# Kernel tuning notes

Measured on AMD Instinct MI355X. Metric: run time of the kernel, lower is better.

The kernel has to match this reference:

```python
import jax, jax.numpy as jnp
import numpy as np

S, B, D, F, E, K = 1024, 2, 512, 2048, 8, 2


def setup_inputs() -> dict:
    key = jax.random.key(0)
    ks = jax.random.split(key, 12)
    s = lambda *sh: 1.0 / np.sqrt(sh[0])
    inp = {
        "x": jax.random.normal(ks[0], (S, B, D), dtype=jnp.float32),
        # gate: nn.Linear(d_model, n_experts)
        "Wg": jax.random.normal(ks[1], (D, E), dtype=jnp.float32) * s(D),
        "bg": jnp.zeros((E,), dtype=jnp.float32),
        # routed experts: stacked FFN params (E copies of expert)
        "W1": jax.random.normal(ks[2], (E, D, F), dtype=jnp.float32) * s(D),
        "b1": jnp.zeros((E, F), dtype=jnp.float32),
        "W2": jax.random.normal(ks[3], (E, F, D), dtype=jnp.float32) * s(F),
        "b2": jnp.zeros((E, D), dtype=jnp.float32),
        # shared expert (single FFN)
        "Ws1": jax.random.normal(ks[4], (D, F), dtype=jnp.float32) * s(D),
        "bs1": jnp.zeros((F,), dtype=jnp.float32),
        "Ws2": jax.random.normal(ks[5], (F, D), dtype=jnp.float32) * s(F),
        "bs2": jnp.zeros((D,), dtype=jnp.float32),
    }
    return inp


def reference(x, Wg, bg, W1, b1, W2, b2, Ws1, bs1, Ws2, bs2):
    # gate_logits: (S, B, E)
    gate_logits = jnp.einsum("sbd,de->sbe", x, Wg) + bg
    # top-k per token (eval mode: k = n_experts_per_token, t = 1.0)
    weights, selected = jax.lax.top_k(gate_logits, K)  # (S,B,K)
    weights = jax.nn.softmax(weights.astype(jnp.float32), axis=-1)
    # combine weights per expert: (S,B,E)
    onehot = jax.nn.one_hot(selected, E, dtype=weights.dtype)  # (S,B,K,E)
    comb = jnp.einsum("sbk,sbke->sbe", weights, onehot)
    # routed experts computed densely, combined with per-token routing weight
    h = jax.nn.relu(jnp.einsum("sbd,edf->sbef", x, W1) + b1)  # (S,B,E,F)
    y = jnp.einsum("sbef,efd->sbed", h, W2) + b2              # (S,B,E,D)
    out = jnp.einsum("sbe,sbed->sbd", comb, y)
    # shared expert, scaled by 1/k
    hs = jax.nn.relu(jnp.einsum("sbd,df->sbf", x, Ws1) + bs1)
    shared = jnp.einsum("sbf,fd->sbd", hs, Ws2) + bs2
    out = out + (1.0 / K) * shared
    return out
```

## Files before the change

### kernel.cpp

```cpp
#include <hip/hip_runtime.h>
#include <hip/hip_bf16.h>
#include <stdint.h>

#define TT 2048
#define DD 512
#define FF 2048
#define EE 8

typedef unsigned short u16;
typedef __attribute__((ext_vector_type(8))) unsigned short ushort8v;
typedef __attribute__((ext_vector_type(8))) short short8;
typedef __attribute__((ext_vector_type(4))) float float4v;

__device__ __forceinline__ u16 f2bf(float f) {
    unsigned u = __float_as_uint(f);
    u += 0x7FFF + ((u >> 16) & 1);
    return (u16)(u >> 16);
}

__device__ __forceinline__ void gl_lds16(const u16* g, u16* l) {
    __builtin_amdgcn_global_load_lds(
        (const __attribute__((address_space(1))) unsigned int*)g,
        (__attribute__((address_space(3))) unsigned int*)l, 16, 0, 0);
}

#define WS_HB   0ull
#define WS_XG   (WS_HB + 6144ull*2048*2)
#define WS_WT1  (WS_XG + 2048ull*512*2)
#define WS_ME   (WS_WT1 + 9ull*2048*512*2)
#define WS_MW   (WS_ME + 16384)
#define WS_RT   (WS_MW + 16384)
#define WS_WROW (WS_RT + 16384)
#define WS_TROW (WS_WROW + 16384)
#define WS_RTG  (WS_TROW + 16384)
#define WS_WT2  (WS_RTG + 128)
#define WS_YB   (WS_WT2 + 9ull*2048*512*2)
#define YS      (6144ull*512)
#define WS_NEED (WS_YB + 2ull*6144*512*4)

__device__ __forceinline__ void conv_unit(int j, const float* __restrict__ srcE,
                                          const float* __restrict__ srcS,
                                          u16* __restrict__ dst,
                                          int R, int C, int shC, u16* Ls) {
    int mid = j >> 8, t2 = j & 255;
    int tr = t2 >> shC, tc = t2 & ((1 << shC) - 1);
    int r0 = tr * 64, c0 = tc * 64;
    const float* src = (mid < 8) ? srcE + (size_t)mid * R * C : srcS;
    u16* dstm = dst + (size_t)mid * R * C;
    int t = threadIdx.x;
#pragma unroll
    for (int i = 0; i < 4; ++i) {
        int rr = (t >> 4) + i * 16;
        int cc = (t & 15) * 4;
        float4v v = *(const float4v*)(src + (size_t)(r0 + rr) * C + c0 + cc);
#pragma unroll
        for (int jx = 0; jx < 4; ++jx) Ls[(cc + jx) * 72 + rr] = f2bf(v[jx]);
    }
    __syncthreads();
#pragma unroll
    for (int jj = 0; jj < 2; ++jj) {
        int slot = t + jj * 256;
        int cc = slot >> 3, r8 = (slot & 7) * 8;
        ushort8v o = *(const ushort8v*)&Ls[cc * 72 + r8];
        *(ushort8v*)(dstm + (size_t)(c0 + cc) * R + r0 + r8) = o;
    }
}

__device__ __forceinline__ void gate_wave(int t, int lane,
                                          const float* __restrict__ x,
                                          const float* __restrict__ Wg,
                                          const float* __restrict__ bg,
                                          int* __restrict__ metaE,
                                          float* __restrict__ metaW,
                                          u16* __restrict__ xg) {
    const float* xp = x + (size_t)t * DD + lane * 8;
    float4v x0 = *(const float4v*)xp;
    float4v x1 = *(const float4v*)(xp + 4);
    float xf[8] = {x0[0], x0[1], x0[2], x0[3], x1[0], x1[1], x1[2], x1[3]};
    float acc[EE] = {0.f, 0.f, 0.f, 0.f, 0.f, 0.f, 0.f, 0.f};
#pragma unroll
    for (int g = 0; g < 8; ++g) {
        const float* wp = Wg + (size_t)(lane * 8 + g) * EE;
        float4v w0 = *(const float4v*)wp;
        float4v w1 = *(const float4v*)(wp + 4);
        acc[0] += xf[g] * w0[0]; acc[1] += xf[g] * w0[1];
        acc[2] += xf[g] * w0[2]; acc[3] += xf[g] * w0[3];
        acc[4] += xf[g] * w1[0]; acc[5] += xf[g] * w1[1];
        acc[6] += xf[g] * w1[2]; acc[7] += xf[g] * w1[3];
    }
#pragma unroll
    for (int off = 1; off < 64; off <<= 1) {
#pragma unroll
        for (int e = 0; e < EE; ++e) acc[e] += __shfl_xor(acc[e], off, 64);
    }
    ushort8v xv;
#pragma unroll
    for (int jx = 0; jx < 4; ++jx) xv[jx] = f2bf(x0[jx]);
#pragma unroll
    for (int jx = 0; jx < 4; ++jx) xv[4 + jx] = f2bf(x1[jx]);
    *(ushort8v*)(xg + (size_t)t * DD + lane * 8) = xv;
    if (lane == 0) {
#pragma unroll
        for (int e = 0; e < EE; ++e) acc[e] += bg[e];
        int e0 = 0; float l0 = acc[0];
#pragma unroll
        for (int e = 1; e < EE; ++e) if (acc[e] > l0) { l0 = acc[e]; e0 = e; }
        int e1 = -1; float l1 = -3.4e38f;
#pragma unroll
        for (int e = 0; e < EE; ++e)
            if (e != e0 && acc[e] > l1) { l1 = acc[e]; e1 = e; }
        float ex = __expf(l1 - l0);
        float w0 = 1.f / (1.f + ex);
        metaE[2 * t] = e0; metaE[2 * t + 1] = e1;
        metaW[2 * t] = w0; metaW[2 * t + 1] = 1.f - w0;
    }
}

__global__ __launch_bounds__(256) void fused1_k(
    const float* __restrict__ x, const float* __restrict__ Wg,
    const float* __restrict__ bg,
    const float* __restrict__ W1, const float* __restrict__ Ws1,
    const float* __restrict__ W2, const float* __restrict__ Ws2,
    float* __restrict__ out, u16* __restrict__ xg,
    u16* __restrict__ Wt1, u16* __restrict__ Wt2,
    int* __restrict__ metaE, float* __restrict__ metaW, int nconv) {
    __shared__ __align__(16) u16 Ls[64 * 72];
    int b = blockIdx.x, tid = threadIdx.x;
    if (b < nconv) {
        if (b < 2304) conv_unit(b, W1, Ws1, Wt1, DD, FF, 5, Ls);
        else          conv_unit(b - 2304, W2, Ws2, Wt2, FF, DD, 3, Ls);
    } else if (b < nconv + 512) {
        int gb = b - nconv;
        gate_wave(gb * 4 + (tid >> 6), tid & 63, x, Wg, bg, metaE, metaW, xg);
    } else {
        int zb = b - nconv - 512;
        float* op = out + (size_t)zb * 8192;
#pragma unroll
        for (int it = 0; it < 8; ++it)
            *(float4v*)(op + it * 1024 + tid * 4) = (float4v){0.f, 0.f, 0.f, 0.f};
    }
}

__global__ __launch_bounds__(256) void conv2_k(const float* __restrict__ W2,
                                               const float* __restrict__ Ws2,
                                               u16* __restrict__ Wt2) {
    __shared__ __align__(16) u16 Ls[64 * 72];
    conv_unit(blockIdx.x, W2, Ws2, Wt2, FF, DD, 3, Ls);
}

__global__ __launch_bounds__(256) void rank_k(const int* __restrict__ metaE,
                                              const float* __restrict__ metaW,
                                              int* __restrict__ routing,
                                              int* __restrict__ rtok,
                                              float* __restrict__ wrow,
                                              int* __restrict__ trow) {
    __shared__ __align__(16) char smem[16384];
    u16* er      = (u16*)smem;
    int* segCnt  = (int*)(smem + 8192);
    int* segBase = (int*)(smem + 10240);
    int* expTot  = (int*)(smem + 12288);
    int tid = threadIdx.x, wv = tid >> 6, lane = tid & 63;
    unsigned long long below = (lane == 0) ? 0ull : ((~0ull) >> (64 - lane));
    for (int s = wv * 16; s < wv * 16 + 16; ++s) {
        int entry = s * 64 + lane;
        int e = metaE[entry];
        int rk = 0;
#pragma unroll
        for (int ee = 0; ee < 8; ++ee) {
            unsigned long long m = __ballot(e == ee);
            if (e == ee) rk = __popcll(m & below);
            if (lane == ee) segCnt[s * 8 + ee] = __popcll(m);
        }
        er[entry] = (u16)(e | (rk << 4));
    }
    __syncthreads();
    if (tid < 8) {
        int s = 0;
        for (int g = 0; g < 64; ++g) { segBase[g * 8 + tid] = s; s += segCnt[g * 8 + tid]; }
        expTot[tid] = s;
    }
    __syncthreads();
    if (tid == 0) {
        int s = 0;
        for (int e = 0; e < 8; ++e) { int c = expTot[e]; expTot[8 + e] = s; s += c; }
    }
    __syncthreads();
    if (tid < 8) { routing[tid] = expTot[8 + tid]; routing[8 + tid] = expTot[tid]; }
    for (int i = 0; i < 16; ++i) {
        int entry = tid + i * 256;
        int v = er[entry];
        int e = v & 15, rk = v >> 4;
        int row = expTot[8 + e] + segBase[(entry >> 6) * 8 + e] + rk;
        rtok[row] = entry >> 1;
        wrow[row] = metaW[entry];
        trow[entry] = row;
    }
}

__global__ __launch_bounds__(256) void gemmA_k(
    const u16* __restrict__ xg, const u16* __restrict__ Wt1,
    const float* __restrict__ b1, const float* __restrict__ bs1,
    const int* __restrict__ routing, const int* __restrict__ rtok,
    u16* __restrict__ hbuf,
    const float* __restrict__ W2, const float* __restrict__ Ws2,
    u16* __restrict__ Wt2, int ncv) {
    __shared__ __align__(16) u16 SM[12288];
    int j = blockIdx.x, tid = threadIdx.x;
    if (j < ncv) { conv_unit(j, W2, Ws2, Wt2, FF, DD, 3, SM); return; }
    j -= ncv;
    u16* As = SM;
    u16* Bs = SM + 4096;
    const int* offs = routing; const int* cnt = routing + 8;
    int rt, ct, Mloc, hRowBase, rowBase; bool routed;
    const u16* Bsrc; const float* bias;
    if (j < 512) {
        rt = j >> 4; ct = j & 15; Mloc = 64; rowBase = rt * 64;
        Bsrc = Wt1 + (size_t)8 * FF * DD; bias = bs1;
        hRowBase = 4096 + rt * 64; routed = false;
    } else {
        int jr = j - 512; int e = jr & 7; int rc = jr >> 3;
        rt = rc >> 4; ct = rc & 15;
        int M = cnt[e]; if (rt * 64 >= M) return;
        Mloc = M - rt * 64; if (Mloc > 64) Mloc = 64;
        rowBase = offs[e] + rt * 64;
        Bsrc = Wt1 + (size_t)e * FF * DD; bias = b1 + e * FF;
        hRowBase = rowBase; routed = true;
    }
    int n0 = ct * 128;
    int lane = tid & 63, w = tid >> 6, ln = lane & 15, quad = lane >> 4;
    int wm = w >> 1, wn = w & 1;
    int lr8 = lane >> 3;
    int cs = (lane & 7) ^ lr8;
    const u16* ApS[2];
#pragma unroll
    for (int i = 0; i < 2; ++i) {
        int r = w * 16 + i * 8 + lr8;
        int tok;
        if (routed) { int br = rowBase + r; if (br > 4095) br = 4095; tok = rtok[br]; }
        else tok = rowBase + r;
        ApS[i] = xg + (size_t)tok * DD + cs * 8;
    }
    const u16* BpS[4];
#pragma unroll
    for (int i = 0; i < 4; ++i) {
        int r = w * 32 + i * 8 + lr8;
        BpS[i] = Bsrc + (size_t)(n0 + r) * DD + cs * 8;
    }
    float4v acc[2][4];
#pragma unroll
    for (int a = 0; a < 2; ++a)
#pragma unroll
        for (int b = 0; b < 4; ++b) acc[a][b] = (float4v){0.f, 0.f, 0.f, 0.f};

#pragma unroll
    for (int kt = 0; kt < 8; ++kt) {
#pragma unroll
        for (int i = 0; i < 2; ++i)
            gl_lds16(ApS[i] + kt * 64, As + (w * 16 + i * 8) * 64);
#pragma unroll
        for (int i = 0; i < 4; ++i)
            gl_lds16(BpS[i] + kt * 64, Bs + (w * 32 + i * 8) * 64);
        asm volatile("s_waitcnt vmcnt(0)" ::: "memory");
        __builtin_amdgcn_s_barrier();
#pragma unroll
        for (int s = 0; s < 2; ++s) {
            int chs = ((s * 4 + quad) ^ (ln & 7)) * 8;
            short8 Af[2], Bf[4];
#pragma unroll
            for (int a = 0; a < 2; ++a) {
                int ra = wm * 32 + a * 16 + ln;
                Af[a] = *(const short8*)(As + ra * 64 + chs);
            }
#pragma unroll
            for (int b = 0; b < 4; ++b) {
                int rb = wn * 64 + b * 16 + ln;
                Bf[b] = *(const short8*)(Bs + rb * 64 + chs);
            }
#pragma unroll
            for (int a = 0; a < 2; ++a)
#pragma unroll
                for (int b = 0; b < 4; ++b)
                    acc[a][b] = __builtin_amdgcn_mfma_f32_16x16x32_bf16(Af[a], Bf[b], acc[a][b], 0, 0, 0);
        }
        __builtin_amdgcn_s_barrier();
    }
#pragma unroll
    for (int b = 0; b < 4; ++b) {
        int n = n0 + wn * 64 + b * 16 + ln;
        float bv = bias[n];
#pragma unroll
        for (int a = 0; a < 2; ++a) {
#pragma unroll
            for (int i = 0; i < 4; ++i) {
                int lr = wm * 32 + a * 16 + quad * 4 + i;
                if (lr < Mloc) {
                    float v = acc[a][b][i] + bv;
                    v = v > 0.f ? v : 0.f;
                    hbuf[(size_t)(hRowBase + lr) * FF + n] = f2bf(v);
                }
            }
        }
    }
}

__global__ __launch_bounds__(256) void gemmB_k(
    const u16* __restrict__ hbuf, const u16* __restrict__ Wt2,
    const float* __restrict__ b2, const float* __restrict__ bs2,
    const int* __restrict__ routing, float* __restrict__ ybuf) {
    __shared__ __align__(16) u16 SM[12288];
    u16* As = SM;
    u16* Bs = SM + 4096;
    const int* offs = routing; const int* cnt = routing + 8;
    int j = blockIdx.x, tid = threadIdx.x;
    int rt, ct, ks, Mloc, aRowBase;
    const u16* Bsrc; const float* bias;
    if (j < 256) {
        rt = j >> 3; ct = (j >> 1) & 3; ks = j & 1;
        Mloc = 64; aRowBase = 4096 + rt * 64;
        Bsrc = Wt2 + (size_t)8 * DD * FF; bias = bs2;
    } else {
        int jr = j - 256; int e = jr & 7; int rc = jr >> 3;
        ks = rc & 1; ct = (rc >> 1) & 3; rt = rc >> 3;
        int M = cnt[e]; if (rt * 64 >= M) return;
        Mloc = M - rt * 64; if (Mloc > 64) Mloc = 64;
        aRowBase = offs[e] + rt * 64;
        Bsrc = Wt2 + (size_t)e * DD * FF; bias = b2 + e * DD;
    }
    int n0 = ct * 128;
    int lane = tid & 63, w = tid >> 6, ln = lane & 15, quad = lane >> 4;
    int wm = w >> 1, wn = w & 1;
    int lr8 = lane >> 3;
    int cs = (lane & 7) ^ lr8;
    const u16* ApS[2];
#pragma unroll
    for (int i = 0; i < 2; ++i) {
        int r = w * 16 + i * 8 + lr8;
        ApS[i] = hbuf + (size_t)(aRowBase + r) * FF + ks * 1024 + cs * 8;
    }
    const u16* BpS[4];
#pragma unroll
    for (int i = 0; i < 4; ++i) {
        int r = w * 32 + i * 8 + lr8;
        BpS[i] = Bsrc + (size_t)(n0 + r) * FF + ks * 1024 + cs * 8;
    }
    float4v acc[2][4];
#pragma unroll
    for (int a = 0; a < 2; ++a)
#pragma unroll
        for (int b = 0; b < 4; ++b) acc[a][b] = (float4v){0.f, 0.f, 0.f, 0.f};

#pragma unroll
    for (int kt = 0; kt < 16; ++kt) {
#pragma unroll
        for (int i = 0; i < 2; ++i)
            gl_lds16(ApS[i] + kt * 64, As + (w * 16 + i * 8) * 64);
#pragma unroll
        for (int i = 0; i < 4; ++i)
            gl_lds16(BpS[i] + kt * 64, Bs + (w * 32 + i * 8) * 64);
        asm volatile("s_waitcnt vmcnt(0)" ::: "memory");
        __builtin_amdgcn_s_barrier();
#pragma unroll
        for (int s = 0; s < 2; ++s) {
            int chs = ((s * 4 + quad) ^ (ln & 7)) * 8;
            short8 Af[2], Bf[4];
#pragma unroll
            for (int a = 0; a < 2; ++a) {
                int ra = wm * 32 + a * 16 + ln;
                Af[a] = *(const short8*)(As + ra * 64 + chs);
            }
#pragma unroll
            for (int b = 0; b < 4; ++b) {
                int rb = wn * 64 + b * 16 + ln;
                Bf[b] = *(const short8*)(Bs + rb * 64 + chs);
            }
#pragma unroll
            for (int a = 0; a < 2; ++a)
#pragma unroll
                for (int b = 0; b < 4; ++b)
                    acc[a][b] = __builtin_amdgcn_mfma_f32_16x16x32_bf16(Af[a], Bf[b], acc[a][b], 0, 0, 0);
        }
        __builtin_amdgcn_s_barrier();
    }
    float* yb = ybuf + (size_t)ks * YS;
#pragma unroll
    for (int b = 0; b < 4; ++b) {
        int n = n0 + wn * 64 + b * 16 + ln;
        float bv = (ks == 0) ? bias[n] : 0.f;
#pragma unroll
        for (int a = 0; a < 2; ++a) {
#pragma unroll
            for (int i = 0; i < 4; ++i) {
                int lr = wm * 32 + a * 16 + quad * 4 + i;
                if (lr < Mloc)
                    yb[(size_t)(aRowBase + lr) * DD + n] = acc[a][b][i] + bv;
            }
        }
    }
}

__global__ __launch_bounds__(256) void combine_k(
    const float* __restrict__ ybuf, const int* __restrict__ trow,
    const float* __restrict__ metaW, float* __restrict__ out) {
    int tid = threadIdx.x;
    int tok = blockIdx.x * 2 + (tid >> 7);
    int q = (tid & 127) * 4;
    int r0 = trow[2 * tok], r1 = trow[2 * tok + 1];
    float w0 = metaW[2 * tok], w1 = metaW[2 * tok + 1];
    const float* ya = ybuf;
    const float* yb = ybuf + YS;
    float4v y0a = *(const float4v*)(ya + (size_t)r0 * DD + q);
    float4v y0b = *(const float4v*)(yb + (size_t)r0 * DD + q);
    float4v y1a = *(const float4v*)(ya + (size_t)r1 * DD + q);
    float4v y1b = *(const float4v*)(yb + (size_t)r1 * DD + q);
    float4v ysa = *(const float4v*)(ya + (size_t)(4096 + tok) * DD + q);
    float4v ysb = *(const float4v*)(yb + (size_t)(4096 + tok) * DD + q);
    float4v o;
#pragma unroll
    for (int i = 0; i < 4; ++i)
        o[i] = w0 * (y0a[i] + y0b[i]) + w1 * (y1a[i] + y1b[i]) + 0.5f * (ysa[i] + ysb[i]);
    *(float4v*)(out + (size_t)tok * DD + q) = o;
}

__global__ __launch_bounds__(256) void gemmBat_k(
    const u16* __restrict__ hbuf, const u16* __restrict__ Wt2,
    const float* __restrict__ b2, const float* __restrict__ bs2,
    const int* __restrict__ routing, const int* __restrict__ rtok,
    const float* __restrict__ wrow, float* __restrict__ out) {
    __shared__ __align__(16) u16 As[2][64 * 64];
    __shared__ __align__(16) u16 Bs[2][128 * 64];
    const int* offs = routing; const int* cnt = routing + 8;
    int j = blockIdx.x, tid = threadIdx.x;
    int rt, ct, ks, Mloc, aRowBase; bool sh;
    const u16* Bsrc; const float* bias;
    if (j < 256) {
        sh = true; rt = j >> 3; int sub = j & 7; ct = sub >> 1; ks = sub & 1;
        Mloc = 64; aRowBase = 4096 + rt * 64;
        Bsrc = Wt2 + (size_t)8 * DD * FF; bias = bs2;
    } else {
        sh = false; int jr = j - 256; int e = jr & 7; int rc = jr >> 3;
        rt = rc >> 3; ct = (rc >> 1) & 3; ks = rc & 1;
        int M = cnt[e]; if (rt * 64 >= M) return;
        Mloc = M - rt * 64; if (Mloc > 64) Mloc = 64;
        aRowBase = offs[e] + rt * 64;
        Bsrc = Wt2 + (size_t)e * DD * FF; bias = b2 + e * DD;
    }
    int n0 = ct * 128;
    int lane = tid & 63, w = tid >> 6, ln = lane & 15, quad = lane >> 4;
    int lr8 = lane >> 3;
    int cs = (lane & 7) ^ lr8;
    const u16* ApS[2];
#pragma unroll
    for (int i = 0; i < 2; ++i) {
        int r = w * 16 + i * 8 + lr8;
        ApS[i] = hbuf + (size_t)(aRowBase + r) * FF + ks * 1024 + cs * 8;
    }
    const u16* BpS[4];
#pragma unroll
    for (int i = 0; i < 4; ++i) {
        int r = w * 32 + i * 8 + lr8;
        BpS[i] = Bsrc + (size_t)(n0 + r) * FF + ks * 1024 + cs * 8;
    }
    float4v acc[2][4];
#pragma unroll
    for (int a = 0; a < 2; ++a)
#pragma unroll
        for (int b = 0; b < 4; ++b) acc[a][b] = (float4v){0.f, 0.f, 0.f, 0.f};
    auto stage = [&](int kt, int pb) {
        u16* Ab = &As[pb][0]; u16* Bb = &Bs[pb][0];
#pragma unroll
        for (int i = 0; i < 2; ++i)
            gl_lds16(ApS[i] + kt * 64, Ab + (w * 16 + i * 8) * 64);
#pragma unroll
        for (int i = 0; i < 4; ++i)
            gl_lds16(BpS[i] + kt * 64, Bb + (w * 32 + i * 8) * 64);
    };
    stage(0, 0);
#pragma unroll
    for (int kt = 0; kt < 16; ++kt) {
        int pb = kt & 1;
        if (kt < 15) {
            stage(kt + 1, pb ^ 1);
            asm volatile("s_waitcnt vmcnt(6)" ::: "memory");
        } else {
            asm volatile("s_waitcnt vmcnt(0)" ::: "memory");
        }
        __builtin_amdgcn_s_barrier();
        __builtin_amdgcn_sched_barrier(0);
        const u16* Ab = &As[pb][0]; const u16* Bb = &Bs[pb][0];
#pragma unroll
        for (int s = 0; s < 2; ++s) {
            int chs = ((s * 4 + quad) ^ (ln & 7)) * 8;
            short8 Af[2], Bf[4];
#pragma unroll
            for (int a = 0; a < 2; ++a) {
                int ra = (w & 1) * 32 + a * 16 + ln;
                Af[a] = *(const short8*)(Ab + ra * 64 + chs);
            }
#pragma unroll
            for (int b = 0; b < 4; ++b) {
                int rb = (w >> 1) * 64 + b * 16 + ln;
                Bf[b] = *(const short8*)(Bb + rb * 64 + chs);
            }
#pragma unroll
            for (int a = 0; a < 2; ++a)
#pragma unroll
                for (int b = 0; b < 4; ++b)
                    acc[a][b] = __builtin_amdgcn_mfma_f32_16x16x32_bf16(Af[a], Bf[b], acc[a][b], 0, 0, 0);
        }
        __builtin_amdgcn_sched_barrier(0);
        __builtin_amdgcn_s_barrier();
    }
    float bv[4];
#pragma unroll
    for (int b = 0; b < 4; ++b)
        bv[b] = (ks == 0) ? bias[n0 + (w >> 1) * 64 + b * 16 + ln] : 0.f;
#pragma unroll
    for (int a = 0; a < 2; ++a) {
#pragma unroll
        for (int i = 0; i < 4; ++i) {
            int lr = (w & 1) * 32 + a * 16 + quad * 4 + i;
            if (lr < Mloc) {
                int row = aRowBase + lr;
                int t; float wr;
                if (sh) { t = row - 4096; wr = 0.5f; }
                else    { t = rtok[row]; wr = wrow[row]; }
                float* op = out + (size_t)t * DD;
#pragma unroll
                for (int b = 0; b < 4; ++b) {
                    int n = n0 + (w >> 1) * 64 + b * 16 + ln;
                    atomicAdd(op + n, wr * (acc[a][b][i] + bv[b]));
                }
            }
        }
    }
}

extern "C" void kernel_launch(void* const* d_in, const int* in_sizes, int n_in,
                              void* d_out, int out_size, void* d_ws, size_t ws_size,
                              hipStream_t stream) {
    const float* x   = (const float*)d_in[0];
    const float* Wg  = (const float*)d_in[1];
    const float* bg  = (const float*)d_in[2];
    const float* W1  = (const float*)d_in[3];
    const float* b1  = (const float*)d_in[4];
    const float* W2  = (const float*)d_in[5];
    const float* b2  = (const float*)d_in[6];
    const float* Ws1 = (const float*)d_in[7];
    const float* bs1 = (const float*)d_in[8];
    const float* Ws2 = (const float*)d_in[9];
    const float* bs2 = (const float*)d_in[10];
    float* out = (float*)d_out;

    char* ws = (char*)d_ws;
    u16*   hbuf    = (u16*)(ws + WS_HB);
    u16*   xg      = (u16*)(ws + WS_XG);
    u16*   Wt1     = (u16*)(ws + WS_WT1);
    int*   metaE   = (int*)(ws + WS_ME);
    float* metaW   = (float*)(ws + WS_MW);
    int*   rtok    = (int*)(ws + WS_RT);
    float* wrow    = (float*)(ws + WS_WROW);
    int*   trow    = (int*)(ws + WS_TROW);
    int*   routing = (int*)(ws + WS_RTG);
    bool   big     = ws_size >= WS_NEED;
    u16*   Wt2     = big ? (u16*)(ws + WS_WT2) : Wt1;
    float* ybuf    = (float*)(ws + WS_YB);

    if (big) {
        fused1_k<<<2816, 256, 0, stream>>>(x, Wg, bg, W1, Ws1, W2, Ws2,
                                           out, xg, Wt1, Wt2, metaE, metaW, 2304);
        rank_k<<<1, 256, 0, stream>>>(metaE, metaW, routing, rtok, wrow, trow);
        gemmA_k<<<2304 + 512 + 8192, 256, 0, stream>>>(
            xg, Wt1, b1, bs1, routing, rtok, hbuf, W2, Ws2, Wt2, 2304);
        gemmB_k<<<256 + 4096, 256, 0, stream>>>(hbuf, Wt2, b2, bs2, routing, ybuf);
        combine_k<<<1024, 256, 0, stream>>>(ybuf, trow, metaW, out);
    } else {
        fused1_k<<<2944, 256, 0, stream>>>(x, Wg, bg, W1, Ws1, W2, Ws2,
                                           out, xg, Wt1, Wt2, metaE, metaW, 2304);
        rank_k<<<1, 256, 0, stream>>>(metaE, metaW, routing, rtok, wrow, trow);
        gemmA_k<<<512 + 8192, 256, 0, stream>>>(
            xg, Wt1, b1, bs1, routing, rtok, hbuf, W2, Ws2, Wt2, 0);
        conv2_k<<<2304, 256, 0, stream>>>(W2, Ws2, Wt2);
        gemmBat_k<<<4352, 256, 0, stream>>>(hbuf, Wt2, b2, bs2, routing, rtok, wrow, out);
    }
}
```

Before: 208.6 us.

## Drop split-K in second expert GEMM and double-buffer its LDS tiles

The second GEMM no longer splits K across two blocks writing separate partial buffers. Each block now loops over the full K with a double-buffered LDS prefetch (waiting on vmcnt(6) so the next tile's loads overlap the current MFMAs), and combine reads one partial instead of two. The weight-conversion transpose also changes its float loads from 4-wide vectors to strided scalars to reduce LDS bank conflicts. This halves the block count and the y-buffer traffic, at the cost of less parallelism per tile and doubled LDS use per block.

```diff
diff --git a/kernel.cpp b/kernel.cpp
--- a/kernel.cpp
+++ b/kernel.cpp
@@ -48,21 +48,22 @@
     const float* src = (mid < 8) ? srcE + (size_t)mid * R * C : srcS;
     u16* dstm = dst + (size_t)mid * R * C;
     int t = threadIdx.x;
+    int cc = t & 15, rbase = t >> 4;
 #pragma unroll
     for (int i = 0; i < 4; ++i) {
-        int rr = (t >> 4) + i * 16;
-        int cc = (t & 15) * 4;
-        float4v v = *(const float4v*)(src + (size_t)(r0 + rr) * C + c0 + cc);
-#pragma unroll
-        for (int jx = 0; jx < 4; ++jx) Ls[(cc + jx) * 72 + rr] = f2bf(v[jx]);
+        int rr = rbase + i * 16;
+        const float* sp = src + (size_t)(r0 + rr) * C + c0 + cc;
+#pragma unroll
+        for (int jx = 0; jx < 4; ++jx)
+            Ls[(cc + 16 * jx) * 72 + rr] = f2bf(sp[16 * jx]);
     }
     __syncthreads();
 #pragma unroll
     for (int jj = 0; jj < 2; ++jj) {
         int slot = t + jj * 256;
-        int cc = slot >> 3, r8 = (slot & 7) * 8;
-        ushort8v o = *(const ushort8v*)&Ls[cc * 72 + r8];
-        *(ushort8v*)(dstm + (size_t)(c0 + cc) * R + r0 + r8) = o;
+        int c2 = slot >> 3, r8 = (slot & 7) * 8;
+        ushort8v o = *(const ushort8v*)&Ls[c2 * 72 + r8];
+        *(ushort8v*)(dstm + (size_t)(c0 + c2) * R + r0 + r8) = o;
     }
 }
 
@@ -307,20 +308,19 @@
     const u16* __restrict__ hbuf, const u16* __restrict__ Wt2,
     const float* __restrict__ b2, const float* __restrict__ bs2,
     const int* __restrict__ routing, float* __restrict__ ybuf) {
-    __shared__ __align__(16) u16 SM[12288];
-    u16* As = SM;
-    u16* Bs = SM + 4096;
+    __shared__ __align__(16) u16 As[2][64 * 64];
+    __shared__ __align__(16) u16 Bs[2][128 * 64];
     const int* offs = routing; const int* cnt = routing + 8;
     int j = blockIdx.x, tid = threadIdx.x;
-    int rt, ct, ks, Mloc, aRowBase;
+    int rt, ct, Mloc, aRowBase;
     const u16* Bsrc; const float* bias;
-    if (j < 256) {
-        rt = j >> 3; ct = (j >> 1) & 3; ks = j & 1;
+    if (j < 128) {
+        rt = j >> 2; ct = j & 3;
         Mloc = 64; aRowBase = 4096 + rt * 64;
         Bsrc = Wt2 + (size_t)8 * DD * FF; bias = bs2;
     } else {
-        int jr = j - 256; int e = jr & 7; int rc = jr >> 3;
-        ks = rc & 1; ct = (rc >> 1) & 3; rt = rc >> 3;
+        int jr = j - 128; int e = jr & 7; int rc = jr >> 3;
+        rt = rc >> 2; ct = rc & 3;
         int M = cnt[e]; if (rt * 64 >= M) return;
         Mloc = M - rt * 64; if (Mloc > 64) Mloc = 64;
         aRowBase = offs[e] + rt * 64;
@@ -328,50 +328,60 @@
     }
     int n0 = ct * 128;
     int lane = tid & 63, w = tid >> 6, ln = lane & 15, quad = lane >> 4;
-    int wm = w >> 1, wn = w & 1;
     int lr8 = lane >> 3;
     int cs = (lane & 7) ^ lr8;
     const u16* ApS[2];
 #pragma unroll
     for (int i = 0; i < 2; ++i) {
         int r = w * 16 + i * 8 + lr8;
-        ApS[i] = hbuf + (size_t)(aRowBase + r) * FF + ks * 1024 + cs * 8;
+        ApS[i] = hbuf + (size_t)(aRowBase + r) * FF + cs * 8;
     }
     const u16* BpS[4];
 #pragma unroll
     for (int i = 0; i < 4; ++i) {
         int r = w * 32 + i * 8 + lr8;
-        BpS[i] = Bsrc + (size_t)(n0 + r) * FF + ks * 1024 + cs * 8;
+        BpS[i] = Bsrc + (size_t)(n0 + r) * FF + cs * 8;
     }
     float4v acc[2][4];
 #pragma unroll
     for (int a = 0; a < 2; ++a)
 #pragma unroll
         for (int b = 0; b < 4; ++b) acc[a][b] = (float4v){0.f, 0.f, 0.f, 0.f};
-
-#pragma unroll
-    for (int kt = 0; kt < 16; ++kt) {
+    auto stage = [&](int kt, int pb) {
+        u16* Ab = &As[pb][0]; u16* Bb = &Bs[pb][0];
 #pragma unroll
         for (int i = 0; i < 2; ++i)
-            gl_lds16(ApS[i] + kt * 64, As + (w * 16 + i * 8) * 64);
+            gl_lds16(ApS[i] + kt * 64, Ab + (w * 16 + i * 8) * 64);
 #pragma unroll
         for (int i = 0; i < 4; ++i)
-            gl_lds16(BpS[i] + kt * 64, Bs + (w * 32 + i * 8) * 64);
-        asm volatile("s_waitcnt vmcnt(0)" ::: "memory");
+            gl_lds16(BpS[i] + kt * 64, Bb + (w * 32 + i * 8) * 64);
+    };
+    stage(0, 0);
+#pragma unroll
+    for (int kt = 0; kt < 32; ++kt) {
+        int pb = kt & 1;
+        if (kt < 31) {
+            stage(kt + 1, pb ^ 1);
+            asm volatile("s_waitcnt vmcnt(6)" ::: "memory");
+        } else {
+            asm volatile("s_waitcnt vmcnt(0)" ::: "memory");
+        }
         __builtin_amdgcn_s_barrier();
+        __builtin_amdgcn_sched_barrier(0);
+        const u16* Ab = &As[pb][0]; const u16* Bb = &Bs[pb][0];
 #pragma unroll
         for (int s = 0; s < 2; ++s) {
             int chs = ((s * 4 + quad) ^ (ln & 7)) * 8;
             short8 Af[2], Bf[4];
 #pragma unroll
             for (int a = 0; a < 2; ++a) {
-                int ra = wm * 32 + a * 16 + ln;
-                Af[a] = *(const short8*)(As + ra * 64 + chs);
+                int ra = (w & 1) * 32 + a * 16 + ln;
+                Af[a] = *(const short8*)(Ab + ra * 64 + chs);
             }
 #pragma unroll
             for (int b = 0; b < 4; ++b) {
-                int rb = wn * 64 + b * 16 + ln;
-                Bf[b] = *(const short8*)(Bs + rb * 64 + chs);
+                int rb = (w >> 1) * 64 + b * 16 + ln;
+                Bf[b] = *(const short8*)(Bb + rb * 64 + chs);
             }
 #pragma unroll
             for (int a = 0; a < 2; ++a)
@@ -379,20 +389,20 @@
                 for (int b = 0; b < 4; ++b)
                     acc[a][b] = __builtin_amdgcn_mfma_f32_16x16x32_bf16(Af[a], Bf[b], acc[a][b], 0, 0, 0);
         }
+        __builtin_amdgcn_sched_barrier(0);
         __builtin_amdgcn_s_barrier();
     }
-    float* yb = ybuf + (size_t)ks * YS;
 #pragma unroll
     for (int b = 0; b < 4; ++b) {
-        int n = n0 + wn * 64 + b * 16 + ln;
-        float bv = (ks == 0) ? bias[n] : 0.f;
+        int n = n0 + (w >> 1) * 64 + b * 16 + ln;
+        float bv = bias[n];
 #pragma unroll
         for (int a = 0; a < 2; ++a) {
 #pragma unroll
             for (int i = 0; i < 4; ++i) {
-                int lr = wm * 32 + a * 16 + quad * 4 + i;
+                int lr = (w & 1) * 32 + a * 16 + quad * 4 + i;
                 if (lr < Mloc)
-                    yb[(size_t)(aRowBase + lr) * DD + n] = acc[a][b][i] + bv;
+                    ybuf[(size_t)(aRowBase + lr) * DD + n] = acc[a][b][i] + bv;
             }
         }
     }
@@ -406,18 +416,12 @@
     int q = (tid & 127) * 4;
     int r0 = trow[2 * tok], r1 = trow[2 * tok + 1];
     float w0 = metaW[2 * tok], w1 = metaW[2 * tok + 1];
-    const float* ya = ybuf;
-    const float* yb = ybuf + YS;
-    float4v y0a = *(const float4v*)(ya + (size_t)r0 * DD + q);
-    float4v y0b = *(const float4v*)(yb + (size_t)r0 * DD + q);
-    float4v y1a = *(const float4v*)(ya + (size_t)r1 * DD + q);
-    float4v y1b = *(const float4v*)(yb + (size_t)r1 * DD + q);
-    float4v ysa = *(const float4v*)(ya + (size_t)(4096 + tok) * DD + q);
-    float4v ysb = *(const float4v*)(yb + (size_t)(4096 + tok) * DD + q);
+    float4v y0 = *(const float4v*)(ybuf + (size_t)r0 * DD + q);
+    float4v y1 = *(const float4v*)(ybuf + (size_t)r1 * DD + q);
+    float4v ys = *(const float4v*)(ybuf + (size_t)(4096 + tok) * DD + q);
     float4v o;
 #pragma unroll
-    for (int i = 0; i < 4; ++i)
-        o[i] = w0 * (y0a[i] + y0b[i]) + w1 * (y1a[i] + y1b[i]) + 0.5f * (ysa[i] + ysb[i]);
+    for (int i = 0; i < 4; ++i) o[i] = w0 * y0[i] + w1 * y1[i] + 0.5f * ys[i];
     *(float4v*)(out + (size_t)tok * DD + q) = o;
 }
 
@@ -571,7 +575,7 @@
         rank_k<<<1, 256, 0, stream>>>(metaE, metaW, routing, rtok, wrow, trow);
         gemmA_k<<<2304 + 512 + 8192, 256, 0, stream>>>(
             xg, Wt1, b1, bs1, routing, rtok, hbuf, W2, Ws2, Wt2, 2304);
-        gemmB_k<<<256 + 4096, 256, 0, stream>>>(hbuf, Wt2, b2, bs2, routing, ybuf);
+        gemmB_k<<<128 + 2048, 256, 0, stream>>>(hbuf, Wt2, b2, bs2, routing, ybuf);
         combine_k<<<1024, 256, 0, stream>>>(ybuf, trow, metaW, out);
     } else {
         fused1_k<<<2944, 256, 0, stream>>>(x, Wg, bg, W1, Ws1, W2, Ws2,
```

Result: no change. 209.4 us (+0.4%).
